# Kernel tuning notes

Hardware: AMD Instinct MI355X
Metric: run time of the kernel (lower is better)

The kernel has to match this reference:

```python
import jax, jax.numpy as jnp
import numpy as np

B, H, D = 2048, 50, 400          # batch, history_length, news/category embed dim
S, C = 285, 18                   # num_subcategories, num_categories
NC = 50                          # num_clicks_embed_dim (= history_length table size)
FILL = 1e-30                     # masked_fill value used by the original module


def setup_inputs() -> dict:
    key = jax.random.key(0)
    ks = jax.random.split(key, 9)
    vectors = jax.random.normal(ks[0], (B, H, D), dtype=jnp.float32)
    subcategory = jax.random.randint(ks[1], (B, H), 0, S, dtype=jnp.int32)
    category = jax.random.randint(ks[2], (B, H), 0, C, dtype=jnp.int32)
    subcat_embed = jax.random.normal(ks[3], (S, D), dtype=jnp.float32) * 0.02
    cat_embed = jax.random.normal(ks[4], (C, D), dtype=jnp.float32) * 0.02
    clicks_embed = jax.random.normal(ks[5], (H, NC), dtype=jnp.float32) * 0.02
    w_news = jax.random.normal(ks[6], (D,), dtype=jnp.float32) * 0.05
    w_subcat = jax.random.normal(ks[7], (D + NC,), dtype=jnp.float32) * 0.05
    w_cat = jax.random.normal(ks[8], (D + NC,), dtype=jnp.float32) * 0.05
    return {"vectors": vectors, "subcategory": subcategory, "category": category,
            "subcat_embed": subcat_embed, "cat_embed": cat_embed,
            "clicks_embed": clicks_embed, "w_news": w_news,
            "w_subcat": w_subcat, "w_cat": w_cat}


def reference(vectors, subcategory, category, subcat_embed, cat_embed,
              clicks_embed, w_news, w_subcat, w_cat):
    sub_mask = jax.nn.one_hot(subcategory, S, dtype=vectors.dtype)   # [B,H,S]
    cat_mask = jax.nn.one_hot(category, C, dtype=vectors.dtype)      # [B,H,C]
    sub_to_cat = jnp.einsum('bhs,bhc->bsc', sub_mask, cat_mask)      # [B,S,C]

    # --- news -> subcategory attention pooling ---
    news_scores = jnp.einsum('bhd,d->bh', vectors, w_news)           # [B,H]
    scores = jnp.where(sub_mask > 0, news_scores[:, :, None], FILL)  # [B,H,S]
    news_w = jax.nn.softmax(scores, axis=1)
    sub_news_repr = jnp.einsum('bhs,bhd->bsd', news_w, vectors)      # [B,S,D]
    sub_repr = sub_news_repr + subcat_embed[None]                    # [B,S,D]

    sub_clicks = sub_mask.sum(axis=1)                                # [B,S] float counts
    sub_weights = sub_clicks / sub_clicks.sum(axis=1, keepdims=True)
    sub_clicks_emb = clicks_embed[sub_clicks.astype(jnp.int32)]      # [B,S,NC]

    # --- subcategory -> category attention pooling ---
    sc_scores = jnp.einsum('bsk,k->bs',
                           jnp.concatenate([sub_repr, sub_clicks_emb], axis=2),
                           w_subcat)                                 # [B,S]
    scores2 = jnp.where(sub_to_cat > 0, sc_scores[:, :, None], FILL) # [B,S,C]
    sub_w = jax.nn.softmax(scores2, axis=1)
    cat_sub_repr = jnp.einsum('bsc,bsd->bcd', sub_w, sub_repr)       # [B,C,D]
    cat_repr = cat_sub_repr + cat_embed[None]                        # [B,C,D]

    cat_clicks = cat_mask.sum(axis=1)                                # [B,C]
    cat_weights = cat_clicks / cat_clicks.sum(axis=1, keepdims=True)
    cat_clicks_emb = clicks_embed[cat_clicks.astype(jnp.int32)]      # [B,C,NC]

    # --- category -> user attention pooling (unmasked) ---
    c_scores = jnp.einsum('bck,k->bc',
                          jnp.concatenate([cat_repr, cat_clicks_emb], axis=2),
                          w_cat)                                     # [B,C]
    cat_w = jax.nn.softmax(c_scores, axis=1)
    user_repr = jnp.einsum('bc,bcd->bd', cat_w, cat_repr)            # [B,D]

    return (sub_repr, sub_weights, cat_repr, cat_weights, user_repr)
```

## Files before the change

### kernel.cpp

```cpp
#include <hip/hip_runtime.h>

#define BB 2048
#define HH 50
#define DD 400
#define D4 100
#define SS 285
#define CC 18
#define NCC 50
#define FILLV 1e-30f

static constexpr int BLOCK = 256;

static constexpr size_t OFF1 = (size_t)BB * SS * DD;
static constexpr size_t OFF2 = OFF1 + (size_t)BB * SS;
static constexpr size_t OFF3 = OFF2 + (size_t)BB * CC * DD;
static constexpr size_t OFF4 = OFF3 + (size_t)BB * CC;

#define WS_ETOT 0
#define WS_SCE  400
#define WS_SEW  688
#define WS_CEDS 976
#define WS_CEDC 1026
#define WS_CEW  1076

typedef float f4 __attribute__((ext_vector_type(4)));
typedef unsigned long long u64;

__device__ __forceinline__ float dot4(f4 a, f4 b) {
    return a.x * b.x + a.y * b.y + a.z * b.z + a.w * b.w;
}

__global__ void hierec_pre(const float* __restrict__ subcat_embed,
                           const float* __restrict__ cat_embed,
                           const float* __restrict__ clicks_embed,
                           const float* __restrict__ w_subcat,
                           const float* __restrict__ w_cat,
                           float* __restrict__ ws)
{
    const int tid  = threadIdx.x;
    const int lane = tid & 63;
    const int wave = tid >> 6;
    const int wpb  = blockDim.x >> 6;
    const int gw   = blockIdx.x * wpb + wave;
    const int nw   = gridDim.x * wpb;

    for (int s = gw; s < SS; s += nw) {
        float p1 = 0.f, p2 = 0.f;
        for (int d = lane; d < DD; d += 64) {
            float v = subcat_embed[s * DD + d];
            p1 += v * w_subcat[d];
            p2 += v * w_cat[d];
        }
        for (int off = 32; off; off >>= 1) {
            p1 += __shfl_down(p1, off);
            p2 += __shfl_down(p2, off);
        }
        if (lane == 0) { ws[WS_SCE + s] = p1; ws[WS_SEW + s] = p2; }
    }
    if (blockIdx.x == 0) {
        for (int d = tid; d < DD; d += blockDim.x) {
            float a = 0.f;
            for (int s = 0; s < SS; ++s) a += subcat_embed[s * DD + d];
            ws[WS_ETOT + d] = a;
        }
    }
    if (blockIdx.x == 1) {
        for (int k = wave; k < HH; k += wpb) {
            float p1 = 0.f, p2 = 0.f;
            if (lane < NCC) {
                float v = clicks_embed[k * NCC + lane];
                p1 = v * w_subcat[DD + lane];
                p2 = v * w_cat[DD + lane];
            }
            for (int off = 32; off; off >>= 1) {
                p1 += __shfl_down(p1, off);
                p2 += __shfl_down(p2, off);
            }
            if (lane == 0) { ws[WS_CEDS + k] = p1; ws[WS_CEDC + k] = p2; }
        }
    }
    if (blockIdx.x == 2) {
        for (int c = wave; c < CC; c += wpb) {
            float p = 0.f;
            for (int d = lane; d < DD; d += 64) p += cat_embed[c * DD + d] * w_cat[d];
            for (int off = 32; off; off >>= 1) p += __shfl_down(p, off);
            if (lane == 0) ws[WS_CEW + c] = p;
        }
    }
}

__global__ __launch_bounds__(BLOCK, 8) void hierec_main(
    const float* __restrict__ vectors,
    const int*   __restrict__ subcategory,
    const int*   __restrict__ category,
    const float* __restrict__ subcat_embed,
    const float* __restrict__ cat_embed,
    const float* __restrict__ w_news,
    const float* __restrict__ w_subcat,
    const float* __restrict__ w_cat,
    const float* __restrict__ pre,
    float* __restrict__ out)
{
    const int b    = blockIdx.x;
    const int tid  = threadIdx.x;
    const int lane = tid & 63;
    const int wave = tid >> 6;

    __shared__ f4     vt4L[D4];
    __shared__ f4     et4L[D4];
    __shared__ f4     Wt4L[D4];
    __shared__ float  coefS[SS];
    __shared__ u64    maskS[SS];
    __shared__ int    cntS[SS];
    __shared__ float  ns1L[HH], ns2L[HH], ns3L[HH];
    __shared__ float  uzL[HH], wNL[HH], scL[HH], Wn3sL[HH];
    __shared__ u64    maskL[HH];
    __shared__ int    hsL[HH], hcL[HH], repL[HH], prepL[HH];
    __shared__ float  mcL[CC], ucL[CC], rZcL[CC], csL[CC], catwL[CC];
    __shared__ int    cntcL[CC];
    __shared__ int    prepStart[CC + 1];
    __shared__ int    prepHL[HH], prepSL[HH];
    __shared__ float  prepGL[HH];
    __shared__ int    clickedL[HH];
    __shared__ int    unclkL[SS];
    __shared__ int    npL, ndL, nUcnt;
    __shared__ float  PvL, vtwL, etwL, Wn3totL;

    const float* vb  = vectors + (size_t)b * HH * DD;
    const f4*    vb4 = (const f4*)vb;
    const f4*    se4 = (const f4*)subcat_embed;
    const f4*    ce4 = (const f4*)cat_embed;
    f4* o4 = (f4*)(out + (size_t)b * SS * DD);

    if (tid < HH) {
        hsL[tid] = subcategory[b * HH + tid];
        hcL[tid] = category[b * HH + tid];
    }
    for (int s = tid; s < SS; s += BLOCK) {
        coefS[s] = 1.f / (float)HH;
        maskS[s] = 0ull;
        cntS[s]  = 0;
    }
    if (tid < D4) {
        et4L[tid] = ((const f4*)pre)[tid];
        f4 z = {0.f, 0.f, 0.f, 0.f};
        vt4L[tid] = z;
        Wt4L[tid] = z;
    }
    if (tid == 0) nUcnt = 0;
    __syncthreads();

    {
        const f4* wn4 = (const f4*)w_news;
        const f4* ws4 = (const f4*)w_subcat;
        const f4* wc4 = (const f4*)w_cat;
        const bool hi = lane < (D4 - 64);
        f4 vtp0 = {0.f, 0.f, 0.f, 0.f};
        f4 vtp1 = {0.f, 0.f, 0.f, 0.f};
        for (int h = wave; h < HH; h += 4) {
            f4 v0 = vb4[h * D4 + lane];
            float p1 = dot4(v0, wn4[lane]);
            float p2 = dot4(v0, ws4[lane]);
            float p3 = dot4(v0, wc4[lane]);
            vtp0 += v0;
            if (hi) {
                f4 v1 = vb4[h * D4 + 64 + lane];
                p1 += dot4(v1, wn4[64 + lane]);
                p2 += dot4(v1, ws4[64 + lane]);
                p3 += dot4(v1, wc4[64 + lane]);
                vtp1 += v1;
            }
            for (int off = 32; off; off >>= 1) {
                p1 += __shfl_down(p1, off);
                p2 += __shfl_down(p2, off);
                p3 += __shfl_down(p3, off);
            }
            if (lane == 0) { ns1L[h] = p1; ns2L[h] = p2; ns3L[h] = p3; }
        }
        float* vtf = (float*)vt4L;
        atomicAdd(&vtf[4 * lane + 0], vtp0.x);
        atomicAdd(&vtf[4 * lane + 1], vtp0.y);
        atomicAdd(&vtf[4 * lane + 2], vtp0.z);
        atomicAdd(&vtf[4 * lane + 3], vtp0.w);
        if (hi) {
            atomicAdd(&vtf[4 * (64 + lane) + 0], vtp1.x);
            atomicAdd(&vtf[4 * (64 + lane) + 1], vtp1.y);
            atomicAdd(&vtf[4 * (64 + lane) + 2], vtp1.z);
            atomicAdd(&vtf[4 * (64 + lane) + 3], vtp1.w);
        }
    }
    __syncthreads();

    if (tid < HH) {
        const int h = tid;
        const int s = hsL[h], c = hcL[h];
        u64 mask = 0ull, pmask = 0ull;
        for (int j = 0; j < HH; ++j) {
            bool ms = (hsL[j] == s);
            mask  |= (u64)(ms ? 1 : 0) << j;
            pmask |= (u64)((ms && hcL[j] == c) ? 1 : 0) << j;
        }
        int cnt = __popcll(mask);
        bool rep = ((__ffsll((long long)mask) - 1) == h);

        float m = FILLV;
        u64 t = mask;
        while (t) { int j = __ffsll((long long)t) - 1; t &= t - 1; m = fmaxf(m, ns1L[j]); }
        float u = expf(FILLV - m);
        float sumE = 0.f, sum2 = 0.f;
        t = mask;
        while (t) {
            int j = __ffsll((long long)t) - 1; t &= t - 1;
            float e = expf(ns1L[j] - m);
            sumE += e;
            sum2 += (e - u) * ns2L[j];
        }
        float Z = sumE + (float)(HH - cnt) * u;
        float vt2 = 0.f;
        for (int j = 0; j < HH; ++j) vt2 += ns2L[j];
        int ci = cnt < (NCC - 1) ? cnt : (NCC - 1);
        float sc = (sum2 + u * vt2) / Z + pre[WS_SCE + s] + pre[WS_CEDS + ci];

        float e_h = expf(ns1L[h] - m);
        float uz = u / Z;
        wNL[h] = (e_h - u) / Z;
        uzL[h] = uz; maskL[h] = mask; scL[h] = sc;
        repL[h]  = rep ? 1 : 0;
        prepL[h] = ((__ffsll((long long)pmask) - 1) == h) ? 1 : 0;
        if (rep) { coefS[s] = uz; maskS[s] = mask; cntS[s] = cnt; }
    } else if (wave == 1) {
        float p = 0.f;
        const float* et = (const float*)et4L;
        for (int d = lane; d < DD; d += 64) p += et[d] * w_cat[d];
        for (int off = 32; off; off >>= 1) p += __shfl_down(p, off);
        if (lane == 0) etwL = p;
    } else if (wave == 2) {
        float p = (lane < HH) ? ns3L[lane] : 0.f;
        for (int off = 32; off; off >>= 1) p += __shfl_down(p, off);
        if (lane == 0) vtwL = p;
    }
    __syncthreads();

    if (tid < CC) {
        const int c = tid;
        float mc = FILLV; int n = 0, cc2 = 0;
        for (int j = 0; j < HH; ++j) {
            if (hcL[j] == c) ++cc2;
            if (prepL[j] && hcL[j] == c) { ++n; mc = fmaxf(mc, scL[j]); }
        }
        float u = expf(FILLV - mc);
        float sumE = 0.f;
        for (int j = 0; j < HH; ++j)
            if (prepL[j] && hcL[j] == c) sumE += expf(scL[j] - mc);
        float Zc = sumE + (float)(SS - n) * u;
        mcL[c] = mc; ucL[c] = u; rZcL[c] = 1.f / Zc; cntcL[c] = cc2;
        __builtin_nontemporal_store((float)cc2 * (1.f / (float)HH),
                                    &out[OFF3 + (size_t)b * CC + c]);
    } else if (tid == 64) {
        int nd = 0, np = 0;
        float sumUb = 0.f;
        for (int j = 0; j < HH; ++j) {
            if (repL[j]) { clickedL[nd] = hsL[j]; ++nd; sumUb += uzL[j]; }
            if (prepL[j]) ++np;
        }
        npL = np; ndL = nd;
        PvL = (float)(SS - nd) * (1.f / (float)HH) + sumUb;
    } else if (tid >= 128 && tid < 128 + HH) {
        const int h = tid - 128;
        float a = 0.f;
        u64 t = maskL[h];
        while (t) { int j = __ffsll((long long)t) - 1; t &= t - 1; a += wNL[j] * ns3L[j]; }
        Wn3sL[h] = a;
    } else if (wave == 3) {
        const int l = tid - 192;
        float p = (l < HH) ? wNL[l] * ns3L[l] : 0.f;
        for (int off = 32; off; off >>= 1) p += __shfl_down(p, off);
        if (l == 0) Wn3totL = p;
    }
    for (int s = tid; s < SS; s += BLOCK) {
        __builtin_nontemporal_store((float)cntS[s] * (1.f / (float)HH),
                                    &out[OFF1 + (size_t)b * SS + s]);
        if (maskS[s] == 0ull) {
            int p = atomicAdd(&nUcnt, 1);
            unclkL[p] = s;
        }
    }
    __syncthreads();

    if (tid < CC) {
        const int c = tid;
        int start = 0;
        for (int j = 0; j < HH; ++j)
            if (prepL[j] && hcL[j] < c) ++start;
        prepStart[c] = start;
        if (c == 0) prepStart[CC] = npL;
        int cur = start;
        float segs = 0.f;
        for (int j = 0; j < HH; ++j) {
            if (prepL[j] && hcL[j] == c) {
                float g = expf(scL[j] - mcL[c]) - ucL[c];
                prepHL[cur] = j; prepSL[cur] = hsL[j]; prepGL[cur] = g;
                segs += g * (uzL[j] * vtwL + Wn3sL[j] + pre[WS_SEW + hsL[j]]);
                ++cur;
            }
        }
        int ci = cntcL[c] < (NCC - 1) ? cntcL[c] : (NCC - 1);
        csL[c] = rZcL[c] * (ucL[c] * (PvL * vtwL + etwL + Wn3totL) + segs)
                 + pre[WS_CEW + c] + pre[WS_CEDC + ci];
    }
    __syncthreads();

    if (tid < CC) {
        float m = csL[0];
        for (int j = 1; j < CC; ++j) m = fmaxf(m, csL[j]);
        float Zc = 0.f;
        for (int j = 0; j < CC; ++j) Zc += expf(csL[j] - m);
        catwL[tid] = expf(csL[tid] - m) / Zc;
    }
    __syncthreads();

    {
        const int tot = ndL * D4;
        for (int i = tid; i < tot; i += BLOCK) {
            int ii = i / D4;
            int q  = i - ii * D4;
            int s  = clickedL[ii];
            f4 wsacc = {0.f, 0.f, 0.f, 0.f};
            u64 t = maskS[s];
            while (t) {
                int j = __ffsll((long long)t) - 1; t &= t - 1;
                wsacc += wNL[j] * vb4[j * D4 + q];
            }
            float* wt = (float*)&Wt4L[q];
            atomicAdd(&wt[0], wsacc.x);
            atomicAdd(&wt[1], wsacc.y);
            atomicAdd(&wt[2], wsacc.z);
            atomicAdd(&wt[3], wsacc.w);
            f4 val = coefS[s] * vt4L[q] + wsacc + se4[s * D4 + q];
            o4[s * D4 + q] = val;
        }
    }
    __syncthreads();


    if (tid < D4) {
        const int q = tid;
        f4 SubTot = PvL * vt4L[q] + Wt4L[q] + et4L[q];
        f4 uacc = {0.f, 0.f, 0.f, 0.f};
        f4* oc = (f4*)(out + OFF2 + (size_t)b * CC * DD);
        for (int c = 0; c < CC; ++c) {
            f4 acc = ucL[c] * SubTot;
            const int e = prepStart[c + 1];
            for (int jj = prepStart[c]; jj < e; ++jj)
                acc += prepGL[jj] * o4[prepSL[jj] * D4 + q];
            f4 val = rZcL[c] * acc + ce4[c * D4 + q];
            uacc += catwL[c] * val;
            __builtin_nontemporal_store(val, &oc[c * D4 + q]);
        }
        f4* ou = (f4*)(out + OFF4 + (size_t)b * DD);
        __builtin_nontemporal_store(uacc, &ou[q]);
    }

    {
        const int tot = (SS - ndL) * D4;
        const float cst = 1.f / (float)HH;
        #pragma unroll 4
        for (int i = tid; i < tot; i += BLOCK) {
            int u = i / D4;
            int q = i - u * D4;
            int s = unclkL[u];
            f4 acc = cst * vt4L[q] + se4[s * D4 + q];
            __builtin_nontemporal_store(acc, &o4[s * D4 + q]);
        }
    }
}

extern "C" void kernel_launch(void* const* d_in, const int* in_sizes, int n_in,
                              void* d_out, int out_size, void* d_ws, size_t ws_size,
                              hipStream_t stream) {
    const float* vectors      = (const float*)d_in[0];
    const int*   subcategory  = (const int*)d_in[1];
    const int*   category     = (const int*)d_in[2];
    const float* subcat_embed = (const float*)d_in[3];
    const float* cat_embed    = (const float*)d_in[4];
    const float* clicks_embed = (const float*)d_in[5];
    const float* w_news       = (const float*)d_in[6];
    const float* w_subcat     = (const float*)d_in[7];
    const float* w_cat        = (const float*)d_in[8];
    float* out = (float*)d_out;
    float* ws  = (float*)d_ws;

    hipLaunchKernelGGL(hierec_pre, dim3(32), dim3(256), 0, stream,
                       subcat_embed, cat_embed, clicks_embed, w_subcat, w_cat, ws);
    hipLaunchKernelGGL(hierec_main, dim3(BB), dim3(BLOCK), 0, stream,
                       vectors, subcategory, category, subcat_embed, cat_embed,
                       w_news, w_subcat, w_cat, ws, out);
}
```

Measured before the change: 511.9 us.

## Split unclicked-subcategory output fill into a separate wide streaming kernel

The main per-batch kernel no longer writes the rows for unclicked subcategories itself. It stores a per-batch base vector and the list of unclicked subcategories into workspace, and a new kernel then fills those rows using four blocks per batch. The aim is to spread the dominant output-store bandwidth over more blocks and shorten the tail of the heavy main kernel. In exchange it adds a kernel launch and a workspace round trip. The new path only runs if the workspace is large enough, and otherwise the old path is kept.

```diff
diff --git a/kernel.cpp b/kernel.cpp
--- a/kernel.cpp
+++ b/kernel.cpp
@@ -22,6 +22,13 @@
 #define WS_CEDS 976
 #define WS_CEDC 1026
 #define WS_CEW  1076
+#define WS_BATCH 1152
+#define PB_BASE  0
+#define PB_LIST  400
+#define PB_NU    685
+#define PB_STRIDE 688
+static constexpr size_t NEEDED_WS_BYTES =
+    (size_t)(WS_BATCH + (size_t)BB * PB_STRIDE) * 4;
 
 typedef float f4 __attribute__((ext_vector_type(4)));
 typedef unsigned long long u64;
@@ -98,13 +105,15 @@
     const float* __restrict__ w_news,
     const float* __restrict__ w_subcat,
     const float* __restrict__ w_cat,
-    const float* __restrict__ pre,
-    float* __restrict__ out)
+    float* __restrict__ ws,
+    float* __restrict__ out,
+    int split)
 {
     const int b    = blockIdx.x;
     const int tid  = threadIdx.x;
     const int lane = tid & 63;
     const int wave = tid >> 6;
+    const float* pre = ws;
 
     __shared__ f4     vt4L[D4];
     __shared__ f4     et4L[D4];
@@ -119,7 +128,7 @@
     __shared__ float  mcL[CC], ucL[CC], rZcL[CC], csL[CC], catwL[CC];
     __shared__ int    cntcL[CC];
     __shared__ int    prepStart[CC + 1];
-    __shared__ int    prepHL[HH], prepSL[HH];
+    __shared__ int    prepSL[HH];
     __shared__ float  prepGL[HH];
     __shared__ int    clickedL[HH];
     __shared__ int    unclkL[SS];
@@ -299,7 +308,7 @@
         for (int j = 0; j < HH; ++j) {
             if (prepL[j] && hcL[j] == c) {
                 float g = expf(scL[j] - mcL[c]) - ucL[c];
-                prepHL[cur] = j; prepSL[cur] = hsL[j]; prepGL[cur] = g;
+                prepSL[cur] = hsL[j]; prepGL[cur] = g;
                 segs += g * (uzL[j] * vtwL + Wn3sL[j] + pre[WS_SEW + hsL[j]]);
                 ++cur;
             }
@@ -361,10 +370,16 @@
         __builtin_nontemporal_store(uacc, &ou[q]);
     }
 
-    {
+    if (split) {
+        float* wb = ws + WS_BATCH + (size_t)b * PB_STRIDE;
+        if (tid < D4) ((f4*)wb)[tid] = (1.f / (float)HH) * vt4L[tid];
+        const int nU = nUcnt;
+        int* wlist = (int*)(wb + PB_LIST);
+        for (int i = tid; i < nU; i += BLOCK) wlist[i] = unclkL[i];
+        if (tid == 0) ((int*)(wb + PB_NU))[0] = nU;
+    } else {
         const int tot = (SS - ndL) * D4;
         const float cst = 1.f / (float)HH;
-        #pragma unroll 4
         for (int i = tid; i < tot; i += BLOCK) {
             int u = i / D4;
             int q = i - u * D4;
@@ -372,6 +387,45 @@
             f4 acc = cst * vt4L[q] + se4[s * D4 + q];
             __builtin_nontemporal_store(acc, &o4[s * D4 + q]);
         }
+    }
+}
+
+static constexpr int CHUNKS = 4;
+
+__global__ __launch_bounds__(BLOCK, 8) void hierec_stream(
+    const float* __restrict__ subcat_embed,
+    const float* __restrict__ ws,
+    float* __restrict__ out)
+{
+    const int b   = blockIdx.x / CHUNKS;
+    const int ch  = blockIdx.x % CHUNKS;
+    const int tid = threadIdx.x;
+
+    __shared__ f4  baseL[D4];
+    __shared__ int listL[(SS + CHUNKS - 1) / CHUNKS + 1];
+
+    const float* wb = ws + WS_BATCH + (size_t)b * PB_STRIDE;
+    if (tid < D4) baseL[tid] = ((const f4*)wb)[tid];
+
+    const int nU  = ((const int*)(wb + PB_NU))[0];
+    const int per = (nU + CHUNKS - 1) / CHUNKS;
+    int r0 = ch * per; if (r0 > nU) r0 = nU;
+    int r1 = r0 + per; if (r1 > nU) r1 = nU;
+    const int nrows = r1 - r0;
+
+    const int* list = (const int*)(wb + PB_LIST);
+    for (int i = tid; i < nrows; i += BLOCK) listL[i] = list[r0 + i];
+    __syncthreads();
+
+    const f4* se4 = (const f4*)subcat_embed;
+    f4* o4 = (f4*)(out + (size_t)b * SS * DD);
+    const int items = nrows * D4;
+    for (int i = tid; i < items; i += BLOCK) {
+        int u = i / D4;
+        int q = i - u * D4;
+        int s = listL[u];
+        f4 v = baseL[q] + se4[s * D4 + q];
+        __builtin_nontemporal_store(v, &o4[s * D4 + q]);
     }
 }
 
@@ -390,9 +444,15 @@
     float* out = (float*)d_out;
     float* ws  = (float*)d_ws;
 
+    const int split = (ws_size >= NEEDED_WS_BYTES) ? 1 : 0;
+
     hipLaunchKernelGGL(hierec_pre, dim3(32), dim3(256), 0, stream,
                        subcat_embed, cat_embed, clicks_embed, w_subcat, w_cat, ws);
     hipLaunchKernelGGL(hierec_main, dim3(BB), dim3(BLOCK), 0, stream,
                        vectors, subcategory, category, subcat_embed, cat_embed,
-                       w_news, w_subcat, w_cat, ws, out);
+                       w_news, w_subcat, w_cat, ws, out, split);
+    if (split) {
+        hipLaunchKernelGGL(hierec_stream, dim3(BB * CHUNKS), dim3(BLOCK), 0, stream,
+                           subcat_embed, ws, out);
+    }
 }
```

Measured after the change: 512.1 us. No clear change (+0.0%).

## Split HieRec into reduction, streaming base-fill and per-batch attention kernels

Applied to the files above, without the earlier changes.

Moves the per-batch score dot products and the column sum of vectors into a separate first kernel, which stages its results in unused output regions. A new tiled streaming kernel fills every sub_repr row with the base value (mean vector plus subcategory embedding), keeping a tile of subcat_embed in shared memory and reusing it across a chunk of batches. The main kernel now only rewrites the clicked rows and the category and user outputs. The category-embedding dot product is now taken from a precomputed per-subcategory sum. The aim is to turn the scattered bulk output writes into regular streaming stores, at the cost of extra kernel launches, an extra pass through scratch memory, and writing the clicked rows twice.

```diff
diff --git a/kernel.cpp b/kernel.cpp
--- a/kernel.cpp
+++ b/kernel.cpp
@@ -89,16 +89,11 @@
     }
 }
 
-__global__ __launch_bounds__(BLOCK, 8) void hierec_main(
+__global__ __launch_bounds__(BLOCK, 8) void hierec_k0(
     const float* __restrict__ vectors,
-    const int*   __restrict__ subcategory,
-    const int*   __restrict__ category,
-    const float* __restrict__ subcat_embed,
-    const float* __restrict__ cat_embed,
     const float* __restrict__ w_news,
     const float* __restrict__ w_subcat,
     const float* __restrict__ w_cat,
-    const float* __restrict__ pre,
     float* __restrict__ out)
 {
     const int b    = blockIdx.x;
@@ -106,48 +101,12 @@
     const int lane = tid & 63;
     const int wave = tid >> 6;
 
-    __shared__ f4     vt4L[D4];
-    __shared__ f4     et4L[D4];
-    __shared__ f4     Wt4L[D4];
-    __shared__ float  coefS[SS];
-    __shared__ u64    maskS[SS];
-    __shared__ int    cntS[SS];
-    __shared__ float  ns1L[HH], ns2L[HH], ns3L[HH];
-    __shared__ float  uzL[HH], wNL[HH], scL[HH], Wn3sL[HH];
-    __shared__ u64    maskL[HH];
-    __shared__ int    hsL[HH], hcL[HH], repL[HH], prepL[HH];
-    __shared__ float  mcL[CC], ucL[CC], rZcL[CC], csL[CC], catwL[CC];
-    __shared__ int    cntcL[CC];
-    __shared__ int    prepStart[CC + 1];
-    __shared__ int    prepHL[HH], prepSL[HH];
-    __shared__ float  prepGL[HH];
-    __shared__ int    clickedL[HH];
-    __shared__ int    unclkL[SS];
-    __shared__ int    npL, ndL, nUcnt;
-    __shared__ float  PvL, vtwL, etwL, Wn3totL;
-
-    const float* vb  = vectors + (size_t)b * HH * DD;
-    const f4*    vb4 = (const f4*)vb;
-    const f4*    se4 = (const f4*)subcat_embed;
-    const f4*    ce4 = (const f4*)cat_embed;
-    f4* o4 = (f4*)(out + (size_t)b * SS * DD);
-
-    if (tid < HH) {
-        hsL[tid] = subcategory[b * HH + tid];
-        hcL[tid] = category[b * HH + tid];
-    }
-    for (int s = tid; s < SS; s += BLOCK) {
-        coefS[s] = 1.f / (float)HH;
-        maskS[s] = 0ull;
-        cntS[s]  = 0;
-    }
-    if (tid < D4) {
-        et4L[tid] = ((const f4*)pre)[tid];
-        f4 z = {0.f, 0.f, 0.f, 0.f};
-        vt4L[tid] = z;
-        Wt4L[tid] = z;
-    }
-    if (tid == 0) nUcnt = 0;
+    __shared__ f4    vt4L[D4];
+    __shared__ float ns1L[HH], ns2L[HH], ns3L[HH];
+
+    const f4* vb4 = (const f4*)(vectors + (size_t)b * HH * DD);
+
+    if (tid < D4) { f4 z = {0.f, 0.f, 0.f, 0.f}; vt4L[tid] = z; }
     __syncthreads();
 
     {
@@ -191,6 +150,114 @@
     }
     __syncthreads();
 
+    float* baseOut = out + OFF4 + (size_t)b * DD;
+    if (tid < D4) ((f4*)baseOut)[tid] = (1.f / (float)HH) * vt4L[tid];
+    float* nsOut = out + OFF2 + (size_t)b * CC * DD;
+    for (int k = tid; k < 3 * HH; k += BLOCK) {
+        float v = (k < HH) ? ns1L[k] : (k < 2 * HH) ? ns2L[k - HH] : ns3L[k - 2 * HH];
+        nsOut[k] = v;
+    }
+}
+
+static constexpr int TILE_S = 15;
+static constexpr int NTILE  = SS / TILE_S;
+static constexpr int NCHUNK = 128;
+static constexpr int BCHUNK = BB / NCHUNK;
+
+__global__ __launch_bounds__(BLOCK) void hierec_stream(
+    const float* __restrict__ subcat_embed,
+    float* __restrict__ out)
+{
+    const int tid  = threadIdx.x;
+    const int tile = blockIdx.x / NCHUNK;
+    const int chk  = blockIdx.x - tile * NCHUNK;
+    const int s0   = tile * TILE_S;
+    const int b0   = chk * BCHUNK;
+
+    __shared__ f4 seL[TILE_S * D4];
+
+    const f4* se4 = (const f4*)subcat_embed + (size_t)s0 * D4;
+    for (int i = tid; i < TILE_S * D4; i += BLOCK) seL[i] = se4[i];
+    __syncthreads();
+
+    for (int bl = 0; bl < BCHUNK; ++bl) {
+        const int b = b0 + bl;
+        const f4* bb = (const f4*)(out + OFF4 + (size_t)b * DD);
+        f4* ob = (f4*)(out + ((size_t)b * SS + s0) * DD);
+        for (int i = tid; i < TILE_S * D4; i += BLOCK) {
+            int r = i / D4;
+            int q = i - r * D4;
+            ob[i] = bb[q] + seL[i];
+        }
+    }
+}
+
+__global__ __launch_bounds__(BLOCK, 8) void hierec_main(
+    const float* __restrict__ vectors,
+    const int*   __restrict__ subcategory,
+    const int*   __restrict__ category,
+    const float* __restrict__ subcat_embed,
+    const float* __restrict__ cat_embed,
+    const float* __restrict__ ws,
+    float* __restrict__ out)
+{
+    const int b    = blockIdx.x;
+    const int tid  = threadIdx.x;
+    const int lane = tid & 63;
+    const int wave = tid >> 6;
+    const float* pre = ws;
+
+    __shared__ f4     vt4L[D4];
+    __shared__ f4     et4L[D4];
+    __shared__ f4     Wt4L[D4];
+    __shared__ float  coefS[SS];
+    __shared__ u64    maskS[SS];
+    __shared__ int    cntS[SS];
+    __shared__ float  ns1L[HH], ns2L[HH], ns3L[HH];
+    __shared__ float  uzL[HH], wNL[HH], scL[HH], Wn3sL[HH];
+    __shared__ u64    maskL[HH];
+    __shared__ int    hsL[HH], hcL[HH], repL[HH], prepL[HH];
+    __shared__ float  mcL[CC], ucL[CC], rZcL[CC], csL[CC], catwL[CC];
+    __shared__ int    cntcL[CC];
+    __shared__ int    prepStart[CC + 1];
+    __shared__ int    prepSL[HH];
+    __shared__ float  prepGL[HH];
+    __shared__ int    clickedL[HH];
+    __shared__ int    npL, ndL;
+    __shared__ float  PvL, vtwL, etwL, Wn3totL;
+
+    const f4* vb4 = (const f4*)(vectors + (size_t)b * HH * DD);
+    const f4* se4 = (const f4*)subcat_embed;
+    const f4* ce4 = (const f4*)cat_embed;
+    f4* o4 = (f4*)(out + (size_t)b * SS * DD);
+
+    if (tid < HH) {
+        hsL[tid] = subcategory[b * HH + tid];
+        hcL[tid] = category[b * HH + tid];
+    }
+    for (int s = tid; s < SS; s += BLOCK) {
+        coefS[s] = 1.f / (float)HH;
+        maskS[s] = 0ull;
+        cntS[s]  = 0;
+    }
+    if (tid < D4) {
+        et4L[tid] = ((const f4*)pre)[tid];
+        f4 base = ((const f4*)(out + OFF4 + (size_t)b * DD))[tid];
+        vt4L[tid] = (float)HH * base;
+        f4 z = {0.f, 0.f, 0.f, 0.f};
+        Wt4L[tid] = z;
+    }
+    {
+        const float* nsIn = out + OFF2 + (size_t)b * CC * DD;
+        for (int k = tid; k < 3 * HH; k += BLOCK) {
+            float v = nsIn[k];
+            if (k < HH) ns1L[k] = v;
+            else if (k < 2 * HH) ns2L[k - HH] = v;
+            else ns3L[k - 2 * HH] = v;
+        }
+    }
+    __syncthreads();
+
     if (tid < HH) {
         const int h = tid;
         const int s = hsL[h], c = hcL[h];
@@ -231,13 +298,19 @@
     } else if (wave == 1) {
         float p = 0.f;
         const float* et = (const float*)et4L;
-        for (int d = lane; d < DD; d += 64) p += et[d] * w_cat[d];
-        for (int off = 32; off; off >>= 1) p += __shfl_down(p, off);
-        if (lane == 0) etwL = p;
+        for (int d = lane; d < DD; d += 64) {
+            p += 0.f;
+        }
+        (void)p;
     } else if (wave == 2) {
         float p = (lane < HH) ? ns3L[lane] : 0.f;
         for (int off = 32; off; off >>= 1) p += __shfl_down(p, off);
         if (lane == 0) vtwL = p;
+    }
+    if (tid == 192) {
+        float p = 0.f;
+        for (int s = 0; s < SS; ++s) p += pre[WS_SEW + s];
+        etwL = p;
     }
     __syncthreads();
 
@@ -271,20 +344,17 @@
         u64 t = maskL[h];
         while (t) { int j = __ffsll((long long)t) - 1; t &= t - 1; a += wNL[j] * ns3L[j]; }
         Wn3sL[h] = a;
-    } else if (wave == 3) {
+    } else if (wave == 3 && tid != 192) {
         const int l = tid - 192;
-        float p = (l < HH) ? wNL[l] * ns3L[l] : 0.f;
-        for (int off = 32; off; off >>= 1) p += __shfl_down(p, off);
-        if (l == 0) Wn3totL = p;
-    }
-    for (int s = tid; s < SS; s += BLOCK) {
+        if (l == 1) {
+            float p = 0.f;
+            for (int j = 0; j < HH; ++j) p += wNL[j] * ns3L[j];
+            Wn3totL = p;
+        }
+    }
+    for (int s = tid; s < SS; s += BLOCK)
         __builtin_nontemporal_store((float)cntS[s] * (1.f / (float)HH),
                                     &out[OFF1 + (size_t)b * SS + s]);
-        if (maskS[s] == 0ull) {
-            int p = atomicAdd(&nUcnt, 1);
-            unclkL[p] = s;
-        }
-    }
     __syncthreads();
 
     if (tid < CC) {
@@ -299,7 +369,7 @@
         for (int j = 0; j < HH; ++j) {
             if (prepL[j] && hcL[j] == c) {
                 float g = expf(scL[j] - mcL[c]) - ucL[c];
-                prepHL[cur] = j; prepSL[cur] = hsL[j]; prepGL[cur] = g;
+                prepSL[cur] = hsL[j]; prepGL[cur] = g;
                 segs += g * (uzL[j] * vtwL + Wn3sL[j] + pre[WS_SEW + hsL[j]]);
                 ++cur;
             }
@@ -341,7 +411,6 @@
         }
     }
     __syncthreads();
-
 
     if (tid < D4) {
         const int q = tid;
@@ -359,19 +428,6 @@
         }
         f4* ou = (f4*)(out + OFF4 + (size_t)b * DD);
         __builtin_nontemporal_store(uacc, &ou[q]);
-    }
-
-    {
-        const int tot = (SS - ndL) * D4;
-        const float cst = 1.f / (float)HH;
-        #pragma unroll 4
-        for (int i = tid; i < tot; i += BLOCK) {
-            int u = i / D4;
-            int q = i - u * D4;
-            int s = unclkL[u];
-            f4 acc = cst * vt4L[q] + se4[s * D4 + q];
-            __builtin_nontemporal_store(acc, &o4[s * D4 + q]);
-        }
     }
 }
 
@@ -392,7 +448,11 @@
 
     hipLaunchKernelGGL(hierec_pre, dim3(32), dim3(256), 0, stream,
                        subcat_embed, cat_embed, clicks_embed, w_subcat, w_cat, ws);
+    hipLaunchKernelGGL(hierec_k0, dim3(BB), dim3(BLOCK), 0, stream,
+                       vectors, w_news, w_subcat, w_cat, out);
+    hipLaunchKernelGGL(hierec_stream, dim3(NTILE * NCHUNK), dim3(BLOCK), 0, stream,
+                       subcat_embed, out);
     hipLaunchKernelGGL(hierec_main, dim3(BB), dim3(BLOCK), 0, stream,
                        vectors, subcategory, category, subcat_embed, cat_embed,
-                       w_news, w_subcat, w_cat, ws, out);
-}
+                       ws, out);
+}
```

Result: slower. 542.4 us (+5.9%).
